# Kernel tuning notes

Measured on AMD Instinct MI355X. Metric: run time of the kernel, lower is better.

Reference implementation:

```python
import jax, jax.numpy as jnp
import numpy as np

B, N_IN, D_IN = 64, 2048, 16
N_OUT, D_OUT = 32, 32
ROUTINGS = 3
EPS = 1e-7


def squash(s, axis=-1):
    # standard CapsNet squash: s * ||s||^2 / (1 + ||s||^2) / ||s||
    sq_norm = jnp.sum(jnp.square(s), axis=axis, keepdims=True)
    scale = sq_norm / (1.0 + sq_norm) / jnp.sqrt(sq_norm + EPS)
    return s * scale


def setup_inputs() -> dict:
    key = jax.random.key(0)
    k1, k2 = jax.random.split(key)
    inputs = jax.random.normal(k1, (B, N_IN, D_IN), dtype=jnp.float32)
    # glorot-uniform-ish scale for [N_out, N_in, D_out, D_in] weight
    limit = np.sqrt(6.0 / (D_IN + D_OUT)).astype(np.float32)
    weight_matrix = jax.random.uniform(k2, (N_OUT, N_IN, D_OUT, D_IN), dtype=jnp.float32,
                                       minval=-limit, maxval=limit)
    return {"inputs": inputs, "weight_matrix": weight_matrix}


def reference(inputs, weight_matrix):
    # u_hat[b,o,i,d] = W[o,i,d,k] @ x[b,i,k]  (replaces tile + map_fn matmul)
    u_hat = jnp.einsum('oidk,bik->boid', weight_matrix, inputs)  # [B, N_out, N_in, D_out]
    b_logits = jnp.zeros((inputs.shape[0], N_OUT, 1, N_IN), dtype=u_hat.dtype)
    v = None
    for r in range(ROUTINGS):
        c = jax.nn.softmax(b_logits, axis=1)                      # softmax over output capsules
        s = jnp.einsum('boli,boid->bold', c, u_hat)               # [B, N_out, 1, D_out]
        v = squash(s)
        if r < ROUTINGS - 1:
            b_logits = b_logits + jnp.einsum('bold,boid->boli', v, u_hat)
    return jnp.squeeze(v, axis=2)                                 # [B, N_out, D_out]
```

## Files before the change

### kernel.cpp

```cpp
#include <hip/hip_runtime.h>

#define B_    64
#define NI    2048
#define DK    16
#define NO    32
#define DOUT  32
#define EPSQ  1e-7f

typedef unsigned u32x2 __attribute__((ext_vector_type(2)));
typedef unsigned u32x4 __attribute__((ext_vector_type(4)));

constexpr int PSEG = 32;

__device__ __forceinline__ unsigned pack2_bf16(float a, float b) {
    unsigned ua = __float_as_uint(a);
    unsigned ub = __float_as_uint(b);
    ua = (ua + 0x7fffu + ((ua >> 16) & 1u)) >> 16;
    ub = (ub + 0x7fffu + ((ub >> 16) & 1u)) >> 16;
    return ua | (ub << 16);
}
__device__ __forceinline__ float bf_lo(unsigned w) { return __uint_as_float(w << 16); }
__device__ __forceinline__ float bf_hi(unsigned w) { return __uint_as_float(w & 0xffff0000u); }


constexpr int WSTRIDE = 516;

__global__ __launch_bounds__(512)
void compute_uhat(const float* __restrict__ x, const float* __restrict__ W,
                  ushort* __restrict__ U)
{
    __shared__ float Ws[NO * WSTRIDE];
    __shared__ float xs[B_ * DK];
    const int i = blockIdx.x;
    const int t = threadIdx.x;

    if (t < 256) {
        const int b = t >> 2, k4 = t & 3;
        float4 v = *(const float4*)(x + ((size_t)b * NI + i) * DK + k4 * 4);
        *(float4*)&xs[b * DK + k4 * 4] = v;
    }

    #pragma unroll
    for (int jj = 0; jj < 8; ++jj) {
        const int p  = t + 512 * jj;
        const int oo = p >> 7;
        const int cc = p & 127;
        float4 v = ((const float4*)(W + ((size_t)oo * NI + i) * (DOUT * DK)))[cc];
        *(float4*)&Ws[oo * WSTRIDE + cc * 4] = v;
    }

    const int o  = t & 31;
    const int q  = (t >> 5) & 7;
    const int bh = t >> 8;

    __syncthreads();

    float w[64];
    {
        const float* wr = &Ws[o * WSTRIDE + q * 64];
        #pragma unroll
        for (int m = 0; m < 16; ++m) {
            float4 v = *(const float4*)(wr + 4 * m);
            w[4*m+0] = v.x; w[4*m+1] = v.y; w[4*m+2] = v.z; w[4*m+3] = v.w;
        }
    }

    const int j = q >> 1, half = q & 1;

    for (int bb = 0; bb < 32; ++bb) {
        const int b = bh * 32 + bb;
        const float4* xv = (const float4*)&xs[b * DK];
        const float4 x0 = xv[0], x1 = xv[1], x2 = xv[2], x3 = xv[3];

        float acc[4];
        #pragma unroll
        for (int dl = 0; dl < 4; ++dl) {
            const float* wr = &w[dl * 16];
            float a;
            a  = wr[0]  * x0.x + wr[1]  * x0.y + wr[2]  * x0.z + wr[3]  * x0.w;
            a += wr[4]  * x1.x + wr[5]  * x1.y + wr[6]  * x1.z + wr[7]  * x1.w;
            a += wr[8]  * x2.x + wr[9]  * x2.y + wr[10] * x2.z + wr[11] * x2.w;
            a += wr[12] * x3.x + wr[13] * x3.y + wr[14] * x3.z + wr[15] * x3.w;
            acc[dl] = a;
        }

        u32x2 pk;
        pk.x = pack2_bf16(acc[0], acc[1]);
        pk.y = pack2_bf16(acc[2], acc[3]);
        const size_t off = ((((size_t)b * NI + i) * 4 + j) * NO + o) * 8 + half * 4;
        __builtin_nontemporal_store(pk, (u32x2*)(U + off));
    }
}

__global__ __launch_bounds__(256)
void sum_u(const ushort* __restrict__ U, float* __restrict__ P0)
{
    __shared__ float red[128 * 9];
    const int t    = threadIdx.x;
    const int b    = blockIdx.x >> 5;
    const int iseg = blockIdx.x & 31;
    const int c    = t & 127;
    const int half = t >> 7;

    float acc[8];
    #pragma unroll
    for (int k = 0; k < 8; ++k) acc[k] = 0.f;

    const u32x4* up = (const u32x4*)U
        + ((size_t)b * NI + (size_t)iseg * (NI / PSEG) + half) * 128 + c;

    #pragma unroll 8
    for (int it = 0; it < (NI / PSEG) / 2; ++it) {
        u32x4 w = __builtin_nontemporal_load(up);
        up += 256;
        acc[0] += bf_lo(w.x); acc[1] += bf_hi(w.x);
        acc[2] += bf_lo(w.y); acc[3] += bf_hi(w.y);
        acc[4] += bf_lo(w.z); acc[5] += bf_hi(w.z);
        acc[6] += bf_lo(w.w); acc[7] += bf_hi(w.w);
    }

    if (half == 1) {
        #pragma unroll
        for (int k = 0; k < 8; ++k) red[c * 9 + k] = acc[k];
    }
    __syncthreads();
    if (half == 0) {
        #pragma unroll
        for (int k = 0; k < 8; ++k) acc[k] = (acc[k] + red[c * 9 + k]) * 0.03125f;

        const int o = c & 31, j = c >> 5;
        float* sp = P0 + ((size_t)(b * PSEG + iseg)) * 1024 + o * 32 + j * 8;
        float4 lo = {acc[0], acc[1], acc[2], acc[3]};
        float4 hi = {acc[4], acc[5], acc[6], acc[7]};
        *(float4*)sp = lo;
        *(float4*)(sp + 4) = hi;
    }
}

template<int R>
__global__ __launch_bounds__(256)
void rsq(const float* __restrict__ P, const float* __restrict__ VsIn,
         float* __restrict__ VsOut)
{
    const int g  = blockIdx.x * 256 + threadIdx.x;
    const int b  = g >> 10, slot = g & 1023;
    float a = 0.f;
    for (int is = 0; is < PSEG; ++is)
        a += P[((size_t)(b * PSEG + is)) * 1024 + slot];

    float sq = a * a;
    #pragma unroll
    for (int msk = 16; msk >= 1; msk >>= 1) sq += __shfl_xor(sq, msk);
    const float sc = sq / (1.f + sq) * rsqrtf(sq + EPSQ);
    const float v  = a * sc;
    VsOut[g] = (R == 1) ? v : v + VsIn[g];
}

__device__ __forceinline__ void mid_proc(const u32x4 c0, const u32x4 c1,
                                         const float* vs, float* sacc)
{
    float lp = 0.f;
    #pragma unroll
    for (int wi = 0; wi < 4; ++wi) {
        lp = fmaf(vs[2*wi],         bf_lo(c0[wi]), lp);
        lp = fmaf(vs[2*wi + 1],     bf_hi(c0[wi]), lp);
        lp = fmaf(vs[8 + 2*wi],     bf_lo(c1[wi]), lp);
        lp = fmaf(vs[8 + 2*wi + 1], bf_hi(c1[wi]), lp);
    }
    lp += __shfl_xor(lp, 32);

    float mx = lp;
    #pragma unroll
    for (int msk = 16; msk >= 1; msk >>= 1) mx = fmaxf(mx, __shfl_xor(mx, msk));
    const float e = __expf(lp - mx);
    float ss = e;
    #pragma unroll
    for (int msk = 16; msk >= 1; msk >>= 1) ss += __shfl_xor(ss, msk);
    const float cc = e / ss;

    #pragma unroll
    for (int wi = 0; wi < 4; ++wi) {
        sacc[2*wi]         = fmaf(cc, bf_lo(c0[wi]), sacc[2*wi]);
        sacc[2*wi + 1]     = fmaf(cc, bf_hi(c0[wi]), sacc[2*wi + 1]);
        sacc[8 + 2*wi]     = fmaf(cc, bf_lo(c1[wi]), sacc[8 + 2*wi]);
        sacc[8 + 2*wi + 1] = fmaf(cc, bf_hi(c1[wi]), sacc[8 + 2*wi + 1]);
    }
}

__global__ __launch_bounds__(256)
void mid(const ushort* __restrict__ U, const float* __restrict__ Vs,
         float* __restrict__ Pout)
{
    __shared__ float sblk[NO * DOUT];
    const int t    = threadIdx.x;
    const int b    = blockIdx.x >> 5;
    const int iseg = blockIdx.x & 31;
    const int i0   = iseg * (NI / PSEG);

    for (int n = t; n < NO * DOUT; n += 256) sblk[n] = 0.f;

    const int lane = t & 63;
    const int o    = lane & 31;
    const int dh   = lane >> 5;
    const int wv   = t >> 6;

    float vs[16];
    {
        const float4* vp = (const float4*)(Vs + ((size_t)b * NO + o) * DOUT + dh * 16);
        #pragma unroll
        for (int m = 0; m < 4; ++m) {
            float4 v = vp[m];
            vs[4*m+0] = v.x; vs[4*m+1] = v.y; vs[4*m+2] = v.z; vs[4*m+3] = v.w;
        }
    }

    float sacc[16];
    #pragma unroll
    for (int ld = 0; ld < 16; ++ld) sacc[ld] = 0.f;

    __syncthreads();

    const u32x4* upA = (const u32x4*)U
        + (((size_t)b * NI + i0 + wv * 16) * 4 + 2 * dh) * NO + o;
    const u32x4* upB = upA + (size_t)8 * 4 * NO;

    u32x4 a0 = __builtin_nontemporal_load(upA);
    u32x4 a1 = __builtin_nontemporal_load(upA + NO);
    u32x4 b0 = __builtin_nontemporal_load(upB);
    u32x4 b1 = __builtin_nontemporal_load(upB + NO);
    upA += 4 * NO;
    upB += 4 * NO;

    for (int ii = 0; ii < 8; ++ii) {
        u32x4 na0 = {}, na1 = {}, nb0 = {}, nb1 = {};
        const bool more = (ii < 7);
        if (more) {
            na0 = __builtin_nontemporal_load(upA);
            na1 = __builtin_nontemporal_load(upA + NO);
            nb0 = __builtin_nontemporal_load(upB);
            nb1 = __builtin_nontemporal_load(upB + NO);
            upA += 4 * NO;
            upB += 4 * NO;
        }

        mid_proc(a0, a1, vs, sacc);
        mid_proc(b0, b1, vs, sacc);

        if (more) { a0 = na0; a1 = na1; b0 = nb0; b1 = nb1; }
    }

    #pragma unroll
    for (int ld = 0; ld < 16; ++ld) {
        const int d = dh * 16 + ld;
        atomicAdd(&sblk[o * 32 + ((d + o) & 31)], sacc[ld]);
    }
    __syncthreads();

    float* sp = Pout + ((size_t)(b * PSEG + iseg)) * 1024;
    for (int n = t; n < NO * DOUT; n += 256) {
        const int oo = n >> 5, dd = n & 31;
        sp[n] = sblk[oo * 32 + ((dd + oo) & 31)];
    }
}

__global__ __launch_bounds__(256)
void squash_final(const float* __restrict__ P2, float* __restrict__ out)
{
    const int g  = blockIdx.x * 256 + threadIdx.x;
    const int b  = g >> 10, slot = g & 1023;
    float a = 0.f;
    for (int is = 0; is < PSEG; ++is)
        a += P2[((size_t)(b * PSEG + is)) * 1024 + slot];

    float sq = a * a;
    #pragma unroll
    for (int msk = 16; msk >= 1; msk >>= 1) sq += __shfl_xor(sq, msk);
    const float sc = sq / (1.f + sq) * rsqrtf(sq + EPSQ);
    out[g] = a * sc;
}

constexpr int BTILE  = 16;
constexpr int ITILE  = 32;
constexpr int CHUNKS = NI / ITILE;
constexpr int GB     = B_ / BTILE;
constexpr int WROW   = DOUT * DK + 4;

__global__ __launch_bounds__(512)
void routing_pass(const float* __restrict__ x, const float* __restrict__ W,
                  const float* __restrict__ Vsum, float* __restrict__ s_out)
{
    __shared__ float W_s[NO * WROW];
    const int tid   = threadIdx.x;
    const int o     = tid & 31;
    const int bl    = tid >> 5;
    const int chunk = blockIdx.x & (CHUNKS - 1);
    const int gb    = blockIdx.x / CHUNKS;
    const int b     = gb * BTILE + bl;

    float vs[DOUT];
    {
        const float4* vp = (const float4*)(Vsum + (size_t)(b * NO + o) * DOUT);
        #pragma unroll
        for (int qq = 0; qq < 8; ++qq) {
            float4 t2 = vp[qq];
            vs[4*qq+0] = t2.x; vs[4*qq+1] = t2.y; vs[4*qq+2] = t2.z; vs[4*qq+3] = t2.w;
        }
    }
    float sacc[DOUT];
    #pragma unroll
    for (int d = 0; d < DOUT; ++d) sacc[d] = 0.f;

    const int o_ld = tid >> 4;
    const int lpos = tid & 15;

    for (int ii = 0; ii < ITILE; ++ii) {
        const int i = chunk * ITILE + ii;
        __syncthreads();
        const float4* wsrc = (const float4*)W + ((size_t)o_ld * NI + i) * (DOUT * DK / 4);
        #pragma unroll
        for (int jj = 0; jj < 8; ++jj) {
            const int f4pos = lpos + 16 * jj;
            float4 v = wsrc[f4pos];
            *(float4*)&W_s[o_ld * WROW + f4pos * 4] = v;
        }
        __syncthreads();

        const float4* xg = (const float4*)(x + ((size_t)b * NI + i) * DK);
        const float4 xr0 = xg[0], xr1 = xg[1], xr2 = xg[2], xr3 = xg[3];

        float u[DOUT];
        float logit = 0.f;
        const float* wrow = &W_s[o * WROW];
        #pragma unroll
        for (int d = 0; d < DOUT; ++d) {
            const float4 w0 = *(const float4*)(wrow + d * DK + 0);
            const float4 w1 = *(const float4*)(wrow + d * DK + 4);
            const float4 w2 = *(const float4*)(wrow + d * DK + 8);
            const float4 w3 = *(const float4*)(wrow + d * DK + 12);
            float acc;
            acc  = w0.x * xr0.x + w0.y * xr0.y + w0.z * xr0.z + w0.w * xr0.w;
            acc += w1.x * xr1.x + w1.y * xr1.y + w1.z * xr1.z + w1.w * xr1.w;
            acc += w2.x * xr2.x + w2.y * xr2.y + w2.z * xr2.z + w2.w * xr2.w;
            acc += w3.x * xr3.x + w3.y * xr3.y + w3.z * xr3.z + w3.w * xr3.w;
            u[d]  = acc;
            logit = fmaf(vs[d], acc, logit);
        }

        float m = logit;
        #pragma unroll
        for (int msk = 16; msk >= 1; msk >>= 1) m = fmaxf(m, __shfl_xor(m, msk));
        const float e = __expf(logit - m);
        float ssum = e;
        #pragma unroll
        for (int msk = 16; msk >= 1; msk >>= 1) ssum += __shfl_xor(ssum, msk);
        const float c = e / ssum;

        #pragma unroll
        for (int d = 0; d < DOUT; ++d) sacc[d] = fmaf(c, u[d], sacc[d]);
    }

    float* sp = s_out + (size_t)(b * NO + o) * DOUT;
    #pragma unroll
    for (int d = 0; d < DOUT; ++d) atomicAdd(&sp[d], sacc[d]);
}

__global__ __launch_bounds__(256)
void squash_update(const float* __restrict__ s, float* __restrict__ Vsum,
                   float* __restrict__ out, int last)
{
    const int tid  = threadIdx.x;
    const int pair = blockIdx.x * 8 + (tid >> 5);
    const int d    = tid & 31;
    const int idx  = pair * DOUT + d;

    const float val = s[idx];
    float sq = val * val;
    #pragma unroll
    for (int msk = 16; msk >= 1; msk >>= 1) sq += __shfl_xor(sq, msk);

    const float scale = sq / (1.f + sq) * rsqrtf(sq + EPSQ);
    const float v = val * scale;

    if (last) out[idx] = v;
    else      Vsum[idx] += v;
}

extern "C" void kernel_launch(void* const* d_in, const int* in_sizes, int n_in,
                              void* d_out, int out_size, void* d_ws, size_t ws_size,
                              hipStream_t stream)
{
    const float* x = (const float*)d_in[0];
    const float* W = (const float*)d_in[1];
    float* out = (float*)d_out;

    const size_t VSB    = (size_t)B_ * 1024 * sizeof(float);
    const size_t PB     = (size_t)B_ * PSEG * 1024 * sizeof(float);
    const size_t UBYTES = (size_t)B_ * NI * NO * DOUT * sizeof(ushort);
    const size_t need   = 2 * VSB + 3 * PB + UBYTES;

    if (ws_size >= need) {
        char* w = (char*)d_ws;
        float* Vs1 = (float*)w;                 w += VSB;
        float* Vs2 = (float*)w;                 w += VSB;
        float* P0  = (float*)w;                 w += PB;
        float* P1  = (float*)w;                 w += PB;
        float* P2  = (float*)w;                 w += PB;
        ushort* U  = (ushort*)w;

        compute_uhat<<<dim3(NI), dim3(512), 0, stream>>>(x, W, U);
        sum_u<<<dim3(B_ * PSEG), dim3(256), 0, stream>>>(U, P0);
        rsq<1><<<dim3(B_ * 1024 / 256), dim3(256), 0, stream>>>(P0, nullptr, Vs1);
        mid<<<dim3(B_ * PSEG), dim3(256), 0, stream>>>(U, Vs1, P1);
        rsq<2><<<dim3(B_ * 1024 / 256), dim3(256), 0, stream>>>(P1, Vs1, Vs2);
        mid<<<dim3(B_ * PSEG), dim3(256), 0, stream>>>(U, Vs2, P2);
        squash_final<<<dim3(B_ * 1024 / 256), dim3(256), 0, stream>>>(P2, out);
    } else {
        float* s0 = (float*)d_ws;
        float* s1 = s0 + (size_t)B_ * 1024;
        hipMemsetAsync(d_ws, 0, (size_t)2 * B_ * 1024 * sizeof(float), stream);
        for (int r = 0; r < 3; ++r) {
            if (r > 0)
                hipMemsetAsync(s0, 0, (size_t)B_ * 1024 * sizeof(float), stream);
            routing_pass<<<dim3(GB * CHUNKS), dim3(512), 0, stream>>>(x, W, s1, s0);
            squash_update<<<dim3(B_ * NO / 8), dim3(256), 0, stream>>>(s0, s1, out, r == 2);
        }
    }
}
```

Measured before the change: 477.1 us.

## Halve partial segments and give each lane a full capsule row in routing

Result: faster. 431.6 us (-9.6%).

```diff
diff --git a/kernel.cpp b/kernel.cpp
--- a/kernel.cpp
+++ b/kernel.cpp
@@ -10,7 +10,7 @@
 typedef unsigned u32x2 __attribute__((ext_vector_type(2)));
 typedef unsigned u32x4 __attribute__((ext_vector_type(4)));
 
-constexpr int PSEG = 32;
+constexpr int PSEG = 16;
 
 __device__ __forceinline__ unsigned pack2_bf16(float a, float b) {
     unsigned ua = __float_as_uint(a);
@@ -97,8 +97,8 @@
 {
     __shared__ float red[128 * 9];
     const int t    = threadIdx.x;
-    const int b    = blockIdx.x >> 5;
-    const int iseg = blockIdx.x & 31;
+    const int b    = blockIdx.x >> 4;
+    const int seg  = blockIdx.x & 15;
     const int c    = t & 127;
     const int half = t >> 7;
 
@@ -107,16 +107,30 @@
     for (int k = 0; k < 8; ++k) acc[k] = 0.f;
 
     const u32x4* up = (const u32x4*)U
-        + ((size_t)b * NI + (size_t)iseg * (NI / PSEG) + half) * 128 + c;
-
-    #pragma unroll 8
-    for (int it = 0; it < (NI / PSEG) / 2; ++it) {
-        u32x4 w = __builtin_nontemporal_load(up);
-        up += 256;
-        acc[0] += bf_lo(w.x); acc[1] += bf_hi(w.x);
-        acc[2] += bf_lo(w.y); acc[3] += bf_hi(w.y);
-        acc[4] += bf_lo(w.z); acc[5] += bf_hi(w.z);
-        acc[6] += bf_lo(w.w); acc[7] += bf_hi(w.w);
+        + ((size_t)b * NI + (size_t)seg * 128 + half * 64) * 128 + c;
+
+    for (int it = 0; it < 16; ++it) {
+        u32x4 w0 = __builtin_nontemporal_load(up);
+        u32x4 w1 = __builtin_nontemporal_load(up + 128);
+        u32x4 w2 = __builtin_nontemporal_load(up + 256);
+        u32x4 w3 = __builtin_nontemporal_load(up + 384);
+        up += 512;
+        acc[0] += bf_lo(w0.x); acc[1] += bf_hi(w0.x);
+        acc[2] += bf_lo(w0.y); acc[3] += bf_hi(w0.y);
+        acc[4] += bf_lo(w0.z); acc[5] += bf_hi(w0.z);
+        acc[6] += bf_lo(w0.w); acc[7] += bf_hi(w0.w);
+        acc[0] += bf_lo(w1.x); acc[1] += bf_hi(w1.x);
+        acc[2] += bf_lo(w1.y); acc[3] += bf_hi(w1.y);
+        acc[4] += bf_lo(w1.z); acc[5] += bf_hi(w1.z);
+        acc[6] += bf_lo(w1.w); acc[7] += bf_hi(w1.w);
+        acc[0] += bf_lo(w2.x); acc[1] += bf_hi(w2.x);
+        acc[2] += bf_lo(w2.y); acc[3] += bf_hi(w2.y);
+        acc[4] += bf_lo(w2.z); acc[5] += bf_hi(w2.z);
+        acc[6] += bf_lo(w2.w); acc[7] += bf_hi(w2.w);
+        acc[0] += bf_lo(w3.x); acc[1] += bf_hi(w3.x);
+        acc[2] += bf_lo(w3.y); acc[3] += bf_hi(w3.y);
+        acc[4] += bf_lo(w3.z); acc[5] += bf_hi(w3.z);
+        acc[6] += bf_lo(w3.w); acc[7] += bf_hi(w3.w);
     }
 
     if (half == 1) {
@@ -129,7 +143,7 @@
         for (int k = 0; k < 8; ++k) acc[k] = (acc[k] + red[c * 9 + k]) * 0.03125f;
 
         const int o = c & 31, j = c >> 5;
-        float* sp = P0 + ((size_t)(b * PSEG + iseg)) * 1024 + o * 32 + j * 8;
+        float* sp = P0 + ((size_t)(b * PSEG + seg)) * 1024 + o * 32 + j * 8;
         float4 lo = {acc[0], acc[1], acc[2], acc[3]};
         float4 hi = {acc[4], acc[5], acc[6], acc[7]};
         *(float4*)sp = lo;
@@ -145,6 +159,7 @@
     const int g  = blockIdx.x * 256 + threadIdx.x;
     const int b  = g >> 10, slot = g & 1023;
     float a = 0.f;
+    #pragma unroll
     for (int is = 0; is < PSEG; ++is)
         a += P[((size_t)(b * PSEG + is)) * 1024 + slot];
 
@@ -156,34 +171,44 @@
     VsOut[g] = (R == 1) ? v : v + VsIn[g];
 }
 
-__device__ __forceinline__ void mid_proc(const u32x4 c0, const u32x4 c1,
-                                         const float* vs, float* sacc)
-{
-    float lp = 0.f;
-    #pragma unroll
-    for (int wi = 0; wi < 4; ++wi) {
-        lp = fmaf(vs[2*wi],         bf_lo(c0[wi]), lp);
-        lp = fmaf(vs[2*wi + 1],     bf_hi(c0[wi]), lp);
-        lp = fmaf(vs[8 + 2*wi],     bf_lo(c1[wi]), lp);
-        lp = fmaf(vs[8 + 2*wi + 1], bf_hi(c1[wi]), lp);
-    }
-    lp += __shfl_xor(lp, 32);
-
-    float mx = lp;
+__device__ __forceinline__ void proc_i(const u32x4* cr, const float* vs, float* sacc)
+{
+    unsigned cw[16];
+    #pragma unroll
+    for (int jj = 0; jj < 4; ++jj) {
+        cw[4*jj+0] = cr[jj].x; cw[4*jj+1] = cr[jj].y;
+        cw[4*jj+2] = cr[jj].z; cw[4*jj+3] = cr[jj].w;
+    }
+
+    float l0 = 0.f, l1 = 0.f, l2 = 0.f, l3 = 0.f;
+    #pragma unroll
+    for (int m = 0; m < 16; m += 4) {
+        const int d0 = (m >> 2) * 8;
+        l0 = fmaf(vs[d0+0], bf_lo(cw[m+0]), l0);
+        l0 = fmaf(vs[d0+1], bf_hi(cw[m+0]), l0);
+        l1 = fmaf(vs[d0+2], bf_lo(cw[m+1]), l1);
+        l1 = fmaf(vs[d0+3], bf_hi(cw[m+1]), l1);
+        l2 = fmaf(vs[d0+4], bf_lo(cw[m+2]), l2);
+        l2 = fmaf(vs[d0+5], bf_hi(cw[m+2]), l2);
+        l3 = fmaf(vs[d0+6], bf_lo(cw[m+3]), l3);
+        l3 = fmaf(vs[d0+7], bf_hi(cw[m+3]), l3);
+    }
+    const float logit = (l0 + l1) + (l2 + l3);
+
+    float mx = logit;
     #pragma unroll
     for (int msk = 16; msk >= 1; msk >>= 1) mx = fmaxf(mx, __shfl_xor(mx, msk));
-    const float e = __expf(lp - mx);
-    float ss = e;
-    #pragma unroll
-    for (int msk = 16; msk >= 1; msk >>= 1) ss += __shfl_xor(ss, msk);
-    const float cc = e / ss;
-
-    #pragma unroll
-    for (int wi = 0; wi < 4; ++wi) {
-        sacc[2*wi]         = fmaf(cc, bf_lo(c0[wi]), sacc[2*wi]);
-        sacc[2*wi + 1]     = fmaf(cc, bf_hi(c0[wi]), sacc[2*wi + 1]);
-        sacc[8 + 2*wi]     = fmaf(cc, bf_lo(c1[wi]), sacc[8 + 2*wi]);
-        sacc[8 + 2*wi + 1] = fmaf(cc, bf_hi(c1[wi]), sacc[8 + 2*wi + 1]);
+    const float e = __expf(logit - mx);
+    float ssum = e;
+    #pragma unroll
+    for (int msk = 16; msk >= 1; msk >>= 1) ssum += __shfl_xor(ssum, msk);
+    const float c = e / ssum;
+
+    #pragma unroll
+    for (int m = 0; m < 16; ++m) {
+        const int d0 = (m >> 2) * 8 + (m & 3) * 2;
+        sacc[d0]     = fmaf(c, bf_lo(cw[m]), sacc[d0]);
+        sacc[d0 + 1] = fmaf(c, bf_hi(cw[m]), sacc[d0 + 1]);
     }
 }
 
@@ -192,71 +217,73 @@
          float* __restrict__ Pout)
 {
     __shared__ float sblk[NO * DOUT];
-    const int t    = threadIdx.x;
-    const int b    = blockIdx.x >> 5;
-    const int iseg = blockIdx.x & 31;
-    const int i0   = iseg * (NI / PSEG);
+    const int t   = threadIdx.x;
+    const int b   = blockIdx.x >> 4;
+    const int seg = blockIdx.x & 15;
+    const int i0  = seg * (NI / PSEG);
+    const int o   = t & 31;
+    const int hw  = t >> 5;
 
     for (int n = t; n < NO * DOUT; n += 256) sblk[n] = 0.f;
 
-    const int lane = t & 63;
-    const int o    = lane & 31;
-    const int dh   = lane >> 5;
-    const int wv   = t >> 6;
-
-    float vs[16];
+    float vs[DOUT];
     {
-        const float4* vp = (const float4*)(Vs + ((size_t)b * NO + o) * DOUT + dh * 16);
-        #pragma unroll
-        for (int m = 0; m < 4; ++m) {
+        const float4* vp = (const float4*)(Vs + ((size_t)b * NO + o) * DOUT);
+        #pragma unroll
+        for (int m = 0; m < 8; ++m) {
             float4 v = vp[m];
             vs[4*m+0] = v.x; vs[4*m+1] = v.y; vs[4*m+2] = v.z; vs[4*m+3] = v.w;
         }
     }
-
-    float sacc[16];
-    #pragma unroll
-    for (int ld = 0; ld < 16; ++ld) sacc[ld] = 0.f;
+    float sacc[DOUT];
+    #pragma unroll
+    for (int d = 0; d < DOUT; ++d) sacc[d] = 0.f;
 
     __syncthreads();
 
-    const u32x4* upA = (const u32x4*)U
-        + (((size_t)b * NI + i0 + wv * 16) * 4 + 2 * dh) * NO + o;
-    const u32x4* upB = upA + (size_t)8 * 4 * NO;
-
-    u32x4 a0 = __builtin_nontemporal_load(upA);
-    u32x4 a1 = __builtin_nontemporal_load(upA + NO);
-    u32x4 b0 = __builtin_nontemporal_load(upB);
-    u32x4 b1 = __builtin_nontemporal_load(upB + NO);
-    upA += 4 * NO;
-    upB += 4 * NO;
+    const u32x4* up = (const u32x4*)U + ((size_t)b * NI + i0 + 2 * hw) * (4 * NO) + o;
+    const size_t step = (size_t)16 * 4 * NO;
+
+    u32x4 cur[8];
+    #pragma unroll
+    for (int jj = 0; jj < 4; ++jj) {
+        cur[jj]     = __builtin_nontemporal_load(up + jj * NO);
+        cur[4 + jj] = __builtin_nontemporal_load(up + 4 * NO + jj * NO);
+    }
+    up += step;
 
     for (int ii = 0; ii < 8; ++ii) {
-        u32x4 na0 = {}, na1 = {}, nb0 = {}, nb1 = {};
+        u32x4 nxt[8] = {};
         const bool more = (ii < 7);
         if (more) {
-            na0 = __builtin_nontemporal_load(upA);
-            na1 = __builtin_nontemporal_load(upA + NO);
-            nb0 = __builtin_nontemporal_load(upB);
-            nb1 = __builtin_nontemporal_load(upB + NO);
-            upA += 4 * NO;
-            upB += 4 * NO;
-        }
-
-        mid_proc(a0, a1, vs, sacc);
-        mid_proc(b0, b1, vs, sacc);
-
-        if (more) { a0 = na0; a1 = na1; b0 = nb0; b1 = nb1; }
-    }
-
-    #pragma unroll
-    for (int ld = 0; ld < 16; ++ld) {
-        const int d = dh * 16 + ld;
-        atomicAdd(&sblk[o * 32 + ((d + o) & 31)], sacc[ld]);
+            #pragma unroll
+            for (int jj = 0; jj < 4; ++jj) {
+                nxt[jj]     = __builtin_nontemporal_load(up + jj * NO);
+                nxt[4 + jj] = __builtin_nontemporal_load(up + 4 * NO + jj * NO);
+            }
+            up += step;
+        }
+
+        proc_i(&cur[0], vs, sacc);
+        proc_i(&cur[4], vs, sacc);
+
+        if (more) {
+            #pragma unroll
+            for (int jj = 0; jj < 8; ++jj) cur[jj] = nxt[jj];
+        }
+    }
+
+    #pragma unroll
+    for (int d = 0; d < DOUT; ++d) sacc[d] += __shfl_xor(sacc[d], 32);
+
+    if ((t & 32) == 0) {
+        #pragma unroll
+        for (int d = 0; d < DOUT; ++d)
+            atomicAdd(&sblk[o * 32 + ((d + o) & 31)], sacc[d]);
     }
     __syncthreads();
 
-    float* sp = Pout + ((size_t)(b * PSEG + iseg)) * 1024;
+    float* sp = Pout + ((size_t)(b * PSEG + seg)) * 1024;
     for (int n = t; n < NO * DOUT; n += 256) {
         const int oo = n >> 5, dd = n & 31;
         sp[n] = sblk[oo * 32 + ((dd + oo) & 31)];
@@ -269,6 +296,7 @@
     const int g  = blockIdx.x * 256 + threadIdx.x;
     const int b  = g >> 10, slot = g & 1023;
     float a = 0.f;
+    #pragma unroll
     for (int is = 0; is < PSEG; ++is)
         a += P2[((size_t)(b * PSEG + is)) * 1024 + slot];
 
```
